# Kernel tuning notes

Hardware: AMD Instinct MI355X
Metric: run time of the kernel (lower is better)

The kernel has to match this reference:

```python
import jax, jax.numpy as jnp
import numpy as np

N_NODES = 50000
N_EDGES = 800000
D_IN = 256
D_HID = 256
N_CLASSES = 32
N_GRAPHS = 64


def _sage_conv(x, src, dst, W_l, b_l, W_r, num_nodes):
    # PyG SAGEConv (mean aggr, root_weight=True):
    # out = lin_l(mean_{j->i} x_j) + lin_r(x_i)
    msg = x[src]                                                   # [E, d]
    agg = jax.ops.segment_sum(msg, dst, num_segments=num_nodes)   # [N, d]
    cnt = jax.ops.segment_sum(jnp.ones((src.shape[0], 1), x.dtype), dst,
                              num_segments=num_nodes)             # [N, 1]
    agg = agg / jnp.maximum(cnt, 1.0)
    return agg @ W_l + b_l + x @ W_r


def setup_inputs() -> dict:
    key = jax.random.key(0)
    ks = jax.random.split(key, 12)
    x = jax.random.normal(ks[0], (N_NODES, D_IN), dtype=jnp.float32)
    edge_index = jax.random.randint(ks[1], (2, N_EDGES), 0, N_NODES, dtype=jnp.int64)
    batch = jnp.sort(jax.random.randint(ks[2], (N_NODES,), 0, N_GRAPHS, dtype=jnp.int64))
    s1 = 1.0 / np.sqrt(D_IN)
    s2 = 1.0 / np.sqrt(D_HID)
    return {
        "x": x,
        "edge_index": edge_index,
        "batch": batch,
        "W1_l": jax.random.uniform(ks[3], (D_IN, D_HID), jnp.float32, -s1, s1),
        "b1": jax.random.uniform(ks[4], (D_HID,), jnp.float32, -s1, s1),
        "W1_r": jax.random.uniform(ks[5], (D_IN, D_HID), jnp.float32, -s1, s1),
        "W2_l": jax.random.uniform(ks[6], (D_HID, D_HID), jnp.float32, -s2, s2),
        "b2": jax.random.uniform(ks[7], (D_HID,), jnp.float32, -s2, s2),
        "W2_r": jax.random.uniform(ks[8], (D_HID, D_HID), jnp.float32, -s2, s2),
        "Wc": jax.random.uniform(ks[9], (D_HID, N_CLASSES), jnp.float32, -s2, s2),
        "bc": jax.random.uniform(ks[10], (N_CLASSES,), jnp.float32, -s2, s2),
    }


def reference(x, edge_index, batch, W1_l, b1, W1_r, W2_l, b2, W2_r, Wc, bc):
    src, dst = edge_index[0], edge_index[1]
    h = jax.nn.relu(_sage_conv(x, src, dst, W1_l, b1, W1_r, N_NODES))
    h = jax.nn.relu(_sage_conv(h, src, dst, W2_l, b2, W2_r, N_NODES))
    # global mean pool over graphs
    gsum = jax.ops.segment_sum(h, batch, num_segments=N_GRAPHS)        # [G, d]
    gcnt = jax.ops.segment_sum(jnp.ones((h.shape[0], 1), h.dtype), batch,
                               num_segments=N_GRAPHS)                  # [G, 1]
    g = gsum / jnp.maximum(gcnt, 1.0)
    return g @ Wc + bc
```

## Files before the change

### kernel.cpp

```cpp
#include <hip/hip_runtime.h>
#include <stdint.h>

#define NNODES 50000
#define NEDGES 800000
#define DDIM 256
#define NCLS 32
#define NGRAPH 64
#define NSCANB ((NNODES + 255) / 256)
#define HISTB ((NEDGES + 255) / 256)
#define HISTB8 (HISTB * 8)
#define CVTXB (NNODES * 64 / 256)
#define CVTWB (2 * 256 * 512 / 256)
#define NPXCD (NNODES / 8)

typedef short bf16x8 __attribute__((ext_vector_type(8)));
typedef float f32x4 __attribute__((ext_vector_type(4)));
typedef unsigned short u16x4 __attribute__((ext_vector_type(4)));
typedef unsigned short u16x8 __attribute__((ext_vector_type(8)));

typedef __attribute__((address_space(1))) const char glb_c;
typedef __attribute__((address_space(3))) char lds_c;


__device__ __forceinline__ unsigned short f2b(float f) {
  uint32_t u = __builtin_bit_cast(uint32_t, f);
  u += 0x7FFFu + ((u >> 16) & 1u);
  return (unsigned short)(u >> 16);
}
__device__ __forceinline__ float b2f(unsigned short u) {
  return __builtin_bit_cast(float, (uint32_t)u << 16);
}
__device__ __forceinline__ float blo(uint32_t u) {
  return __builtin_bit_cast(float, u << 16);
}
__device__ __forceinline__ float bhi(uint32_t u) {
  return __builtin_bit_cast(float, u & 0xFFFF0000u);
}

__device__ __forceinline__ void gload16(const void* g, const void* l) {
  __builtin_amdgcn_global_load_lds((glb_c*)g, (lds_c*)l, 16, 0, 0);
}


__global__ void k_hist(const int* __restrict__ dst, int* __restrict__ cnt) {
  int b = blockIdx.x;
  int xcd = b & 7;
  int e = (b >> 3) * 256 + threadIdx.x;
  if (e < NEDGES) {
    int d = dst[e];
    if ((unsigned)(d - xcd * NPXCD) < (unsigned)NPXCD) atomicAdd(&cnt[d], 1);
  }
}

__global__ void k_scan1(const int* __restrict__ cnt, int* __restrict__ bsum) {
  int b = blockIdx.x;
  int i = b * 256 + threadIdx.x;
  int lane = threadIdx.x & 63, wid = threadIdx.x >> 6;
  int v = (i < NNODES) ? cnt[i] : 0;
#pragma unroll
  for (int o = 1; o < 64; o <<= 1) v += __shfl_xor(v, o, 64);
  __shared__ int ws[4];
  if (lane == 0) ws[wid] = v;
  __syncthreads();
  if (threadIdx.x == 0) bsum[b] = ws[0] + ws[1] + ws[2] + ws[3];
}

__global__ void k_scan2(const int* __restrict__ bsum, int* __restrict__ boffs) {
  int tid = threadIdx.x, lane = tid & 63, wid = tid >> 6;
  int v = (tid < NSCANB) ? bsum[tid] : 0;
  int s = v;
#pragma unroll
  for (int o = 1; o < 64; o <<= 1) {
    int t = __shfl_up(s, o, 64);
    if (lane >= o) s += t;
  }
  __shared__ int ws[4];
  if (lane == 63) ws[wid] = s;
  __syncthreads();
  int add = 0;
  for (int w = 0; w < wid; ++w) add += ws[w];
  if (tid < NSCANB) boffs[tid] = s + add - v;
}

__global__ void k_scan3(const int* __restrict__ cnt, const int* __restrict__ boffs,
                        int* __restrict__ rowptr, int* __restrict__ cursor,
                        float* __restrict__ gsum, const int* __restrict__ batch,
                        int* __restrict__ gcnt) {
  int b = blockIdx.x;
  if (b < NSCANB) {
    int i = b * 256 + threadIdx.x;
    int lane = threadIdx.x & 63, wid = threadIdx.x >> 6;
    int v = (i < NNODES) ? cnt[i] : 0;
    int s = v;
#pragma unroll
    for (int o = 1; o < 64; o <<= 1) {
      int t = __shfl_up(s, o, 64);
      if (lane >= o) s += t;
    }
    __shared__ int ws[4];
    if (lane == 63) ws[wid] = s;
    __syncthreads();
    int add = boffs[b];
    for (int w = 0; w < wid; ++w) add += ws[w];
    int incl = s + add;
    if (i < NNODES) {
      rowptr[i + 1] = incl;
      cursor[i] = incl - v;
    }
    if (b == 0 && threadIdx.x == 0) rowptr[0] = 0;
  } else if (b == NSCANB) {
    for (int i = threadIdx.x; i < NGRAPH * DDIM; i += 256) gsum[i] = 0.f;
  } else {
    int g = threadIdx.x;
    if (g < NGRAPH) {
      int lo = 0, hi = NNODES;
      while (lo < hi) { int m = (lo + hi) >> 1; if (batch[m] < g) lo = m + 1; else hi = m; }
      int lo2 = lo, hi2 = NNODES;
      while (lo2 < hi2) { int m = (lo2 + hi2) >> 1; if (batch[m] < g + 1) lo2 = m + 1; else hi2 = m; }
      gcnt[g] = lo2 - lo;
    }
  }
}


__global__ void k_fillcvt(const int* __restrict__ src, const int* __restrict__ dst,
                          int* __restrict__ cursor, int* __restrict__ col,
                          const float* __restrict__ x, unsigned short* __restrict__ xb,
                          const float* __restrict__ W1l, const float* __restrict__ W1r,
                          const float* __restrict__ W2l, const float* __restrict__ W2r,
                          unsigned short* __restrict__ WT1, unsigned short* __restrict__ WT2) {
  int b = blockIdx.x;
  if (b < HISTB8) {
    int xcd = b & 7;
    int e = (b >> 3) * 256 + threadIdx.x;
    if (e < NEDGES) {
      int d = dst[e];
      if ((unsigned)(d - xcd * NPXCD) < (unsigned)NPXCD) {
        int p = atomicAdd(&cursor[d], 1);
        col[p] = src[e] * 32;
      }
    }
  } else if (b < HISTB8 + CVTXB) {
    int i = (b - HISTB8) * 256 + threadIdx.x;
    int r = i >> 6, c4 = i & 63;
    float4 v = *(const float4*)(x + (size_t)r * DDIM + c4 * 4);
    u16x4 o;
    o.x = f2b(v.x); o.y = f2b(v.y); o.z = f2b(v.z); o.w = f2b(v.w);
    int slab = c4 >> 3, seg = c4 & 7;
    *(u16x4*)(xb + ((size_t)slab * NNODES + r) * 32 + seg * 4) = o;
  } else {
    int idx = (b - HISTB8 - CVTXB) * 256 + threadIdx.x;
    int which = idx >> 17;
    int id2 = idx & 131071;
    int n = id2 >> 9, k = id2 & 511;
    const float* Wl = which ? W2l : W1l;
    const float* Wr = which ? W2r : W1r;
    unsigned short* WT = which ? WT2 : WT1;
    float v = (k < 256) ? Wl[k * 256 + n] : Wr[(k - 256) * 256 + n];
    WT[id2] = f2b(v);
  }
}


__global__ void k_agg(const unsigned short* __restrict__ feat,
                      const int* __restrict__ rowptr, const int* __restrict__ col,
                      unsigned short* __restrict__ out) {
  int g = blockIdx.x & 7;
  int nb = blockIdx.x >> 3;
  int wv = threadIdx.x >> 6, lane = threadIdx.x & 63;
  int ns = lane >> 2;
  int seg = lane & 3;
  int node = nb * 64 + wv * 16 + ns;
  bool valid = node < NNODES;
  int nn = valid ? node : NNODES - 1;
  int s = rowptr[nn], e = rowptr[nn + 1];
  if (!valid) e = s;
  const unsigned short* slabp = feat + (size_t)g * NNODES * 32 + seg * 8;
  float a[8] = {0.f}, bb[8] = {0.f};
  int i = s;
  for (; i + 8 <= e; i += 8) {
    uint4 vv[8];
#pragma unroll
    for (int j = 0; j < 8; ++j) {
      int ce = col[i + j];
      vv[j] = *(const uint4*)(slabp + (size_t)ce);
    }
#pragma unroll
    for (int j = 0; j < 8; j += 2) {
      a[0] += blo(vv[j].x); a[1] += bhi(vv[j].x);
      a[2] += blo(vv[j].y); a[3] += bhi(vv[j].y);
      a[4] += blo(vv[j].z); a[5] += bhi(vv[j].z);
      a[6] += blo(vv[j].w); a[7] += bhi(vv[j].w);
      bb[0] += blo(vv[j + 1].x); bb[1] += bhi(vv[j + 1].x);
      bb[2] += blo(vv[j + 1].y); bb[3] += bhi(vv[j + 1].y);
      bb[4] += blo(vv[j + 1].z); bb[5] += bhi(vv[j + 1].z);
      bb[6] += blo(vv[j + 1].w); bb[7] += bhi(vv[j + 1].w);
    }
  }
  if (i < e) {
    int last = e - 1;
    uint4 vv[8];
#pragma unroll
    for (int j = 0; j < 8; ++j) {
      int idx = i + j;
      int cidx = (idx <= last) ? idx : last;
      int ce = col[cidx];
      uint4 r = *(const uint4*)(slabp + (size_t)ce);
      if (idx > last) { r.x = 0u; r.y = 0u; r.z = 0u; r.w = 0u; }
      vv[j] = r;
    }
#pragma unroll
    for (int j = 0; j < 8; j += 2) {
      a[0] += blo(vv[j].x); a[1] += bhi(vv[j].x);
      a[2] += blo(vv[j].y); a[3] += bhi(vv[j].y);
      a[4] += blo(vv[j].z); a[5] += bhi(vv[j].z);
      a[6] += blo(vv[j].w); a[7] += bhi(vv[j].w);
      bb[0] += blo(vv[j + 1].x); bb[1] += bhi(vv[j + 1].x);
      bb[2] += blo(vv[j + 1].y); bb[3] += bhi(vv[j + 1].y);
      bb[4] += blo(vv[j + 1].z); bb[5] += bhi(vv[j + 1].z);
      bb[6] += blo(vv[j + 1].w); bb[7] += bhi(vv[j + 1].w);
    }
  }
  if (valid) {
    float inv = (e > s) ? 1.f / (float)(e - s) : 0.f;
    u16x8 o;
#pragma unroll
    for (int j = 0; j < 8; ++j) o[j] = f2b((a[j] + bb[j]) * inv);
    unsigned short* op = out + ((size_t)g * NNODES + node) * 32 + seg * 8;
    __builtin_nontemporal_store(o, (u16x8*)op);
  }
}


__global__ void k_gemm(const unsigned short* __restrict__ Aagg,
                       const unsigned short* __restrict__ Aroot,
                       const unsigned short* __restrict__ WT,
                       const float* __restrict__ bias,
                       unsigned short* __restrict__ out) {
  __shared__ unsigned short As[128 * 32];
  __shared__ unsigned short Bs[256 * 32];
  int m0 = blockIdx.x * 128;
  int tid = threadIdx.x, lane = tid & 63, wv = tid >> 6;
  int wm = wv >> 1, wn = wv & 1;

  f32x4 acc[2][8];
#pragma unroll
  for (int m = 0; m < 2; ++m)
#pragma unroll
    for (int n = 0; n < 8; ++n) acc[m][n] = (f32x4)0.f;

  for (int kt = 0; kt < 16; ++kt) {
    int k = kt * 32;
    const unsigned short* Abase = (kt < 8) ? Aagg : Aroot;
    int slab = kt & 7;
    const unsigned short* Aslab = Abase + (size_t)slab * NNODES * 32;
    {
      int row = tid >> 2, sg = tid & 3;
      int gr = m0 + row;
      if (gr >= NNODES) gr = NNODES - 1;
      const unsigned short* sp = Aslab + (size_t)gr * 32 + sg * 8;
      gload16(sp, (const char*)As + (wv * 64) * 16);
    }
#pragma unroll
    for (int p = 0; p < 2; ++p) {
      int idx = p * 512 + tid;
      int row = idx >> 2, sg = idx & 3;
      const unsigned short* sp = WT + (size_t)row * 512 + k + sg * 8;
      gload16(sp, (const char*)Bs + (p * 512 + wv * 64) * 16);
    }
    __syncthreads();

    bf16x8 af[2], bfr[8];
    int kb = (lane >> 4) * 8;
    int rA = wm * 32 + (lane & 15);
    int rB = wn * 128 + (lane & 15);
#pragma unroll
    for (int m = 0; m < 2; ++m) af[m] = *(const bf16x8*)&As[(rA + m * 16) * 32 + kb];
#pragma unroll
    for (int n = 0; n < 8; ++n) bfr[n] = *(const bf16x8*)&Bs[(rB + n * 16) * 32 + kb];
#pragma unroll
    for (int m = 0; m < 2; ++m)
#pragma unroll
      for (int n = 0; n < 8; ++n)
        acc[m][n] = __builtin_amdgcn_mfma_f32_16x16x32_bf16(af[m], bfr[n], acc[m][n], 0, 0, 0);
    __syncthreads();
  }

  int rbase = m0 + wm * 32 + (lane >> 4) * 4;
  int cb = wn * 128 + (lane & 15);
#pragma unroll
  for (int n = 0; n < 8; ++n) {
    int cc = cb + n * 16;
    float bv = bias[cc];
    size_t sbase = (size_t)(cc >> 5) * NNODES * 32 + (cc & 31);
#pragma unroll
    for (int m = 0; m < 2; ++m) {
#pragma unroll
      for (int j = 0; j < 4; ++j) {
        int r = rbase + m * 16 + j;
        if (r < NNODES) {
          float v = acc[m][n][j] + bv;
          v = fmaxf(v, 0.f);
          out[sbase + (size_t)r * 32] = f2b(v);
        }
      }
    }
  }
}


#define GSUM_WAVES 1024
__global__ void k_gsum(const unsigned short* __restrict__ h2,
                       const int* __restrict__ batch,
                       float* __restrict__ gsum) {
  int wave = (blockIdx.x * blockDim.x + threadIdx.x) >> 6;
  int lane = threadIdx.x & 63;
  const int per = (NNODES + GSUM_WAVES - 1) / GSUM_WAVES;
  int r0 = wave * per;
  int r1 = r0 + per; if (r1 > NNODES) r1 = NNODES;
  if (r0 >= r1) return;
  int slab = lane >> 3, seg = lane & 7;
  int cb = slab * 32 + seg * 4;
  const unsigned short* sp = h2 + (size_t)slab * NNODES * 32 + seg * 4;
  float a0 = 0.f, a1 = 0.f, a2 = 0.f, a3 = 0.f;
  int cur = batch[r0];
  for (int r = r0; r < r1; ++r) {
    int g = batch[r];
    if (g != cur) {
      float* gp = gsum + cur * DDIM + cb;
      atomicAdd(gp + 0, a0); atomicAdd(gp + 1, a1);
      atomicAdd(gp + 2, a2); atomicAdd(gp + 3, a3);
      a0 = a1 = a2 = a3 = 0.f;
      cur = g;
    }
    u16x4 v = *(const u16x4*)(sp + (size_t)r * 32);
    a0 += b2f(v.x); a1 += b2f(v.y); a2 += b2f(v.z); a3 += b2f(v.w);
  }
  float* gp = gsum + cur * DDIM + cb;
  atomicAdd(gp + 0, a0); atomicAdd(gp + 1, a1);
  atomicAdd(gp + 2, a2); atomicAdd(gp + 3, a3);
}

__global__ void k_cls(const float* __restrict__ gsum, const int* __restrict__ cnt,
                      const float* __restrict__ Wc, const float* __restrict__ bc,
                      float* __restrict__ out) {
  int g = blockIdx.x;
  __shared__ float colmean[DDIM];
  int c = threadIdx.x;
  int n = cnt[g];
  float inv = (n > 0) ? 1.f / (float)n : 0.f;
  colmean[c] = gsum[g * DDIM + c] * inv;
  __syncthreads();
  if (c < NCLS) {
    float o = bc[c];
#pragma unroll 4
    for (int k = 0; k < DDIM; ++k) o += colmean[k] * Wc[k * NCLS + c];
    out[g * NCLS + c] = o;
  }
}


extern "C" void kernel_launch(void* const* d_in, const int* in_sizes, int n_in,
                              void* d_out, int out_size, void* d_ws, size_t ws_size,
                              hipStream_t stream) {
  const float* x    = (const float*)d_in[0];
  const int* eidx   = (const int*)d_in[1];
  const int* batch  = (const int*)d_in[2];
  const float* W1l  = (const float*)d_in[3];
  const float* b1   = (const float*)d_in[4];
  const float* W1r  = (const float*)d_in[5];
  const float* W2l  = (const float*)d_in[6];
  const float* b2   = (const float*)d_in[7];
  const float* W2r  = (const float*)d_in[8];
  const float* Wc   = (const float*)d_in[9];
  const float* bc   = (const float*)d_in[10];
  float* out = (float*)d_out;

  const int* esrc = eidx;
  const int* edst = eidx + NEDGES;

  char* w = (char*)d_ws;
  size_t off = 0;
  auto alloc = [&](size_t bytes) -> char* {
    char* p = w + off;
    off = (off + bytes + 255) & ~(size_t)255;
    return p;
  };
  int* rowptr = (int*)alloc((NNODES + 1) * sizeof(int));
  int* cnt    = (int*)alloc(NNODES * sizeof(int));
  int* cursor = (int*)alloc(NNODES * sizeof(int));
  int* col    = (int*)alloc(NEDGES * sizeof(int));
  unsigned short* xb   = (unsigned short*)alloc((size_t)NNODES * DDIM * 2);
  unsigned short* h1b  = (unsigned short*)alloc((size_t)NNODES * DDIM * 2);
  unsigned short* aggb = (unsigned short*)alloc((size_t)NNODES * DDIM * 2);
  unsigned short* WT1  = (unsigned short*)alloc(512 * 256 * 2);
  unsigned short* WT2  = (unsigned short*)alloc(512 * 256 * 2);
  float* gsum = (float*)alloc(NGRAPH * DDIM * sizeof(float));
  int* gcnt   = (int*)alloc(NGRAPH * sizeof(int));
  int* bsum   = (int*)alloc(NSCANB * sizeof(int));
  int* boffs  = (int*)alloc(NSCANB * sizeof(int));

  hipMemsetAsync(cnt, 0, NNODES * sizeof(int), stream);
  k_hist<<<HISTB8, 256, 0, stream>>>(edst, cnt);
  k_scan1<<<NSCANB, 256, 0, stream>>>(cnt, bsum);
  k_scan2<<<1, 256, 0, stream>>>(bsum, boffs);
  k_scan3<<<NSCANB + 2, 256, 0, stream>>>(cnt, boffs, rowptr, cursor,
                                          gsum, batch, gcnt);
  k_fillcvt<<<HISTB8 + CVTXB + CVTWB, 256, 0, stream>>>(esrc, edst, cursor, col,
                                                        x, xb, W1l, W1r, W2l, W2r,
                                                        WT1, WT2);

  int ggrid = (NNODES + 127) / 128;
  int agg_grid = ((NNODES + 63) / 64) * 8;

  k_agg<<<agg_grid, 256, 0, stream>>>(xb, rowptr, col, aggb);
  k_gemm<<<ggrid, 512, 0, stream>>>(aggb, xb, WT1, b1, h1b);

  k_agg<<<agg_grid, 256, 0, stream>>>(h1b, rowptr, col, aggb);
  k_gemm<<<ggrid, 512, 0, stream>>>(aggb, h1b, WT2, b2, xb);

  k_gsum<<<GSUM_WAVES / 4, 256, 0, stream>>>(xb, batch, gsum);
  k_cls<<<NGRAPH, 256, 0, stream>>>(gsum, gcnt, Wc, bc, out);
}
```

Baseline: 290.7 us.

## Overlap root-weight GEMM with neighbor aggregation in one fused launch

Splits each SAGE layer's GEMM into a root part (x @ W_r + b), computed by extra blocks in the same launch as the gather-aggregation, and a left part (agg @ W_l) that adds the precomputed root result before ReLU. The compute-bound root GEMM is meant to run concurrently with the memory-bound gather and halve the K loop of the post-aggregation GEMM. In exchange it writes and reads an extra bf16 N×256 intermediate, rounding it to bf16 before the add, and the combined-kernel LDS use can cut occupancy for the aggregation blocks.

```diff
diff --git a/kernel.cpp b/kernel.cpp
--- a/kernel.cpp
+++ b/kernel.cpp
@@ -12,6 +12,8 @@
 #define CVTXB (NNODES * 64 / 256)
 #define CVTWB (2 * 256 * 512 / 256)
 #define NPXCD (NNODES / 8)
+#define AGGB (((NNODES + 63) / 64) * 8)
+#define ROOTB (((NNODES + 127) / 128) * 2)
 
 typedef short bf16x8 __attribute__((ext_vector_type(8)));
 typedef float f32x4 __attribute__((ext_vector_type(4)));
@@ -162,81 +164,154 @@
 }
 
 
-__global__ void k_agg(const unsigned short* __restrict__ feat,
-                      const int* __restrict__ rowptr, const int* __restrict__ col,
-                      unsigned short* __restrict__ out) {
-  int g = blockIdx.x & 7;
-  int nb = blockIdx.x >> 3;
-  int wv = threadIdx.x >> 6, lane = threadIdx.x & 63;
-  int ns = lane >> 2;
-  int seg = lane & 3;
-  int node = nb * 64 + wv * 16 + ns;
-  bool valid = node < NNODES;
-  int nn = valid ? node : NNODES - 1;
-  int s = rowptr[nn], e = rowptr[nn + 1];
-  if (!valid) e = s;
-  const unsigned short* slabp = feat + (size_t)g * NNODES * 32 + seg * 8;
-  float a[8] = {0.f}, bb[8] = {0.f};
-  int i = s;
-  for (; i + 8 <= e; i += 8) {
-    uint4 vv[8];
-#pragma unroll
-    for (int j = 0; j < 8; ++j) {
-      int ce = col[i + j];
-      vv[j] = *(const uint4*)(slabp + (size_t)ce);
-    }
-#pragma unroll
-    for (int j = 0; j < 8; j += 2) {
-      a[0] += blo(vv[j].x); a[1] += bhi(vv[j].x);
-      a[2] += blo(vv[j].y); a[3] += bhi(vv[j].y);
-      a[4] += blo(vv[j].z); a[5] += bhi(vv[j].z);
-      a[6] += blo(vv[j].w); a[7] += bhi(vv[j].w);
-      bb[0] += blo(vv[j + 1].x); bb[1] += bhi(vv[j + 1].x);
-      bb[2] += blo(vv[j + 1].y); bb[3] += bhi(vv[j + 1].y);
-      bb[4] += blo(vv[j + 1].z); bb[5] += bhi(vv[j + 1].z);
-      bb[6] += blo(vv[j + 1].w); bb[7] += bhi(vv[j + 1].w);
-    }
-  }
-  if (i < e) {
-    int last = e - 1;
-    uint4 vv[8];
-#pragma unroll
-    for (int j = 0; j < 8; ++j) {
-      int idx = i + j;
-      int cidx = (idx <= last) ? idx : last;
-      int ce = col[cidx];
-      uint4 r = *(const uint4*)(slabp + (size_t)ce);
-      if (idx > last) { r.x = 0u; r.y = 0u; r.z = 0u; r.w = 0u; }
-      vv[j] = r;
-    }
-#pragma unroll
-    for (int j = 0; j < 8; j += 2) {
-      a[0] += blo(vv[j].x); a[1] += bhi(vv[j].x);
-      a[2] += blo(vv[j].y); a[3] += bhi(vv[j].y);
-      a[4] += blo(vv[j].z); a[5] += bhi(vv[j].z);
-      a[6] += blo(vv[j].w); a[7] += bhi(vv[j].w);
-      bb[0] += blo(vv[j + 1].x); bb[1] += bhi(vv[j + 1].x);
-      bb[2] += blo(vv[j + 1].y); bb[3] += bhi(vv[j + 1].y);
-      bb[4] += blo(vv[j + 1].z); bb[5] += bhi(vv[j + 1].z);
-      bb[6] += blo(vv[j + 1].w); bb[7] += bhi(vv[j + 1].w);
-    }
-  }
-  if (valid) {
-    float inv = (e > s) ? 1.f / (float)(e - s) : 0.f;
-    u16x8 o;
-#pragma unroll
-    for (int j = 0; j < 8; ++j) o[j] = f2b((a[j] + bb[j]) * inv);
-    unsigned short* op = out + ((size_t)g * NNODES + node) * 32 + seg * 8;
-    __builtin_nontemporal_store(o, (u16x8*)op);
-  }
-}
-
-
-__global__ void k_gemm(const unsigned short* __restrict__ Aagg,
-                       const unsigned short* __restrict__ Aroot,
-                       const unsigned short* __restrict__ WT,
-                       const float* __restrict__ bias,
-                       unsigned short* __restrict__ out) {
+__global__ void k_aggroot(const unsigned short* __restrict__ feat,
+                          const int* __restrict__ rowptr, const int* __restrict__ col,
+                          unsigned short* __restrict__ aggout,
+                          const unsigned short* __restrict__ WT,
+                          const float* __restrict__ bias,
+                          unsigned short* __restrict__ Crow) {
+  __shared__ unsigned short As[128 * 32];
+  __shared__ unsigned short Bs[128 * 32];
+  int b = blockIdx.x;
+  if (b < AGGB) {
+    int g = b & 7;
+    int nb = b >> 3;
+    int wv = threadIdx.x >> 6, lane = threadIdx.x & 63;
+    int ns = lane >> 2;
+    int seg = lane & 3;
+    int node = nb * 64 + wv * 16 + ns;
+    bool valid = node < NNODES;
+    int nn = valid ? node : NNODES - 1;
+    int s = rowptr[nn], e = rowptr[nn + 1];
+    if (!valid) e = s;
+    const unsigned short* slabp = feat + (size_t)g * NNODES * 32 + seg * 8;
+    float a[8] = {0.f}, bb[8] = {0.f};
+    int i = s;
+    for (; i + 8 <= e; i += 8) {
+      uint4 vv[8];
+#pragma unroll
+      for (int j = 0; j < 8; ++j) {
+        int ce = col[i + j];
+        vv[j] = *(const uint4*)(slabp + (size_t)ce);
+      }
+#pragma unroll
+      for (int j = 0; j < 8; j += 2) {
+        a[0] += blo(vv[j].x); a[1] += bhi(vv[j].x);
+        a[2] += blo(vv[j].y); a[3] += bhi(vv[j].y);
+        a[4] += blo(vv[j].z); a[5] += bhi(vv[j].z);
+        a[6] += blo(vv[j].w); a[7] += bhi(vv[j].w);
+        bb[0] += blo(vv[j + 1].x); bb[1] += bhi(vv[j + 1].x);
+        bb[2] += blo(vv[j + 1].y); bb[3] += bhi(vv[j + 1].y);
+        bb[4] += blo(vv[j + 1].z); bb[5] += bhi(vv[j + 1].z);
+        bb[6] += blo(vv[j + 1].w); bb[7] += bhi(vv[j + 1].w);
+      }
+    }
+    if (i < e) {
+      int last = e - 1;
+      uint4 vv[8];
+#pragma unroll
+      for (int j = 0; j < 8; ++j) {
+        int idx = i + j;
+        int cidx = (idx <= last) ? idx : last;
+        int ce = col[cidx];
+        uint4 r = *(const uint4*)(slabp + (size_t)ce);
+        if (idx > last) { r.x = 0u; r.y = 0u; r.z = 0u; r.w = 0u; }
+        vv[j] = r;
+      }
+#pragma unroll
+      for (int j = 0; j < 8; j += 2) {
+        a[0] += blo(vv[j].x); a[1] += bhi(vv[j].x);
+        a[2] += blo(vv[j].y); a[3] += bhi(vv[j].y);
+        a[4] += blo(vv[j].z); a[5] += bhi(vv[j].z);
+        a[6] += blo(vv[j].w); a[7] += bhi(vv[j].w);
+        bb[0] += blo(vv[j + 1].x); bb[1] += bhi(vv[j + 1].x);
+        bb[2] += blo(vv[j + 1].y); bb[3] += bhi(vv[j + 1].y);
+        bb[4] += blo(vv[j + 1].z); bb[5] += bhi(vv[j + 1].z);
+        bb[6] += blo(vv[j + 1].w); bb[7] += bhi(vv[j + 1].w);
+      }
+    }
+    if (valid) {
+      float inv = (e > s) ? 1.f / (float)(e - s) : 0.f;
+      u16x8 o;
+#pragma unroll
+      for (int j = 0; j < 8; ++j) o[j] = f2b((a[j] + bb[j]) * inv);
+      unsigned short* op = aggout + ((size_t)g * NNODES + node) * 32 + seg * 8;
+      __builtin_nontemporal_store(o, (u16x8*)op);
+    }
+  } else {
+    int gb = b - AGGB;
+    int m0 = (gb >> 1) * 128;
+    int n0 = (gb & 1) * 128;
+    int tid = threadIdx.x, lane = tid & 63, wv = tid >> 6;
+    int wm = wv >> 1, wn = wv & 1;
+
+    f32x4 acc[4][4];
+#pragma unroll
+    for (int m = 0; m < 4; ++m)
+#pragma unroll
+      for (int n = 0; n < 4; ++n) acc[m][n] = (f32x4)0.f;
+
+    for (int kt = 8; kt < 16; ++kt) {
+      int k = kt * 32;
+      int slab = kt & 7;
+      const unsigned short* Aslab = feat + (size_t)slab * NNODES * 32;
+#pragma unroll
+      for (int q = 0; q < 2; ++q) {
+        int idx = q * 256 + tid;
+        int row = idx >> 2, sg = idx & 3;
+        int gr = m0 + row;
+        if (gr >= NNODES) gr = NNODES - 1;
+        const unsigned short* sp = Aslab + (size_t)gr * 32 + sg * 8;
+        gload16(sp, (const char*)As + (q * 256 + wv * 64) * 16);
+      }
+#pragma unroll
+      for (int q = 0; q < 2; ++q) {
+        int idx = q * 256 + tid;
+        int row = idx >> 2, sg = idx & 3;
+        const unsigned short* sp = WT + (size_t)(n0 + row) * 512 + k + sg * 8;
+        gload16(sp, (const char*)Bs + (q * 256 + wv * 64) * 16);
+      }
+      __syncthreads();
+
+      bf16x8 af[4], bfr[4];
+      int kb = (lane >> 4) * 8;
+      int rA = wm * 64 + (lane & 15);
+      int rB = wn * 64 + (lane & 15);
+#pragma unroll
+      for (int m = 0; m < 4; ++m) af[m] = *(const bf16x8*)&As[(rA + m * 16) * 32 + kb];
+#pragma unroll
+      for (int n = 0; n < 4; ++n) bfr[n] = *(const bf16x8*)&Bs[(rB + n * 16) * 32 + kb];
+#pragma unroll
+      for (int m = 0; m < 4; ++m)
+#pragma unroll
+        for (int n = 0; n < 4; ++n)
+          acc[m][n] = __builtin_amdgcn_mfma_f32_16x16x32_bf16(af[m], bfr[n], acc[m][n], 0, 0, 0);
+      __syncthreads();
+    }
+
+    int rbase = m0 + wm * 64 + (lane >> 4) * 4;
+    int cbase = n0 + wn * 64 + (lane & 15);
+#pragma unroll
+    for (int n = 0; n < 4; ++n) {
+      int cc = cbase + n * 16;
+      float bv = bias[cc];
+#pragma unroll
+      for (int m = 0; m < 4; ++m) {
+#pragma unroll
+        for (int j = 0; j < 4; ++j) {
+          int r = rbase + m * 16 + j;
+          if (r < NNODES) Crow[(size_t)r * DDIM + cc] = f2b(acc[m][n][j] + bv);
+        }
+      }
+    }
+  }
+}
+
+
+__global__ void k_lgemm(const unsigned short* __restrict__ Aagg,
+                        const unsigned short* __restrict__ WT,
+                        const unsigned short* __restrict__ Crow,
+                        unsigned short* __restrict__ out) {
   __shared__ unsigned short As[128 * 32];
   __shared__ unsigned short Bs[256 * 32];
   int m0 = blockIdx.x * 128;
@@ -249,11 +324,9 @@
 #pragma unroll
     for (int n = 0; n < 8; ++n) acc[m][n] = (f32x4)0.f;
 
-  for (int kt = 0; kt < 16; ++kt) {
+  for (int kt = 0; kt < 8; ++kt) {
     int k = kt * 32;
-    const unsigned short* Abase = (kt < 8) ? Aagg : Aroot;
-    int slab = kt & 7;
-    const unsigned short* Aslab = Abase + (size_t)slab * NNODES * 32;
+    const unsigned short* Aslab = Aagg + (size_t)kt * NNODES * 32;
     {
       int row = tid >> 2, sg = tid & 3;
       int gr = m0 + row;
@@ -291,7 +364,6 @@
 #pragma unroll
   for (int n = 0; n < 8; ++n) {
     int cc = cb + n * 16;
-    float bv = bias[cc];
     size_t sbase = (size_t)(cc >> 5) * NNODES * 32 + (cc & 31);
 #pragma unroll
     for (int m = 0; m < 2; ++m) {
@@ -299,7 +371,7 @@
       for (int j = 0; j < 4; ++j) {
         int r = rbase + m * 16 + j;
         if (r < NNODES) {
-          float v = acc[m][n][j] + bv;
+          float v = acc[m][n][j] + b2f(Crow[(size_t)r * DDIM + cc]);
           v = fmaxf(v, 0.f);
           out[sbase + (size_t)r * 32] = f2b(v);
         }
@@ -393,6 +465,7 @@
   unsigned short* xb   = (unsigned short*)alloc((size_t)NNODES * DDIM * 2);
   unsigned short* h1b  = (unsigned short*)alloc((size_t)NNODES * DDIM * 2);
   unsigned short* aggb = (unsigned short*)alloc((size_t)NNODES * DDIM * 2);
+  unsigned short* crow = (unsigned short*)alloc((size_t)NNODES * DDIM * 2);
   unsigned short* WT1  = (unsigned short*)alloc(512 * 256 * 2);
   unsigned short* WT2  = (unsigned short*)alloc(512 * 256 * 2);
   float* gsum = (float*)alloc(NGRAPH * DDIM * sizeof(float));
@@ -410,14 +483,13 @@
                                                         x, xb, W1l, W1r, W2l, W2r,
                                                         WT1, WT2);
 
-  int ggrid = (NNODES + 127) / 128;
-  int agg_grid = ((NNODES + 63) / 64) * 8;
-
-  k_agg<<<agg_grid, 256, 0, stream>>>(xb, rowptr, col, aggb);
-  k_gemm<<<ggrid, 512, 0, stream>>>(aggb, xb, WT1, b1, h1b);
-
-  k_agg<<<agg_grid, 256, 0, stream>>>(h1b, rowptr, col, aggb);
-  k_gemm<<<ggrid, 512, 0, stream>>>(aggb, h1b, WT2, b2, xb);
+  int lgrid = (NNODES + 127) / 128;
+
+  k_aggroot<<<AGGB + ROOTB, 256, 0, stream>>>(xb, rowptr, col, aggb, WT1, b1, crow);
+  k_lgemm<<<lgrid, 512, 0, stream>>>(aggb, WT1, crow, h1b);
+
+  k_aggroot<<<AGGB + ROOTB, 256, 0, stream>>>(h1b, rowptr, col, aggb, WT2, b2, crow);
+  k_lgemm<<<lgrid, 512, 0, stream>>>(aggb, WT2, crow, xb);
 
   k_gsum<<<GSUM_WAVES / 4, 256, 0, stream>>>(xb, batch, gsum);
   k_cls<<<NGRAPH, 256, 0, stream>>>(gsum, gcnt, Wc, bc, out);
```

Result: slower. 333.5 us (+14.7%).
